# Kernel optimization log

Hardware: AMD Instinct MI355X
Metric: run time of the kernel (lower is better)

Reference implementation:

```python
import jax, jax.numpy as jnp
import numpy as np

N_STEPS = 20      # max(n_steps_al, n_steps_kc)
ALPHA   = 0.9     # membrane decay exp(-dt/tau_m)
V_TH    = 1.0     # spiking threshold
G_SOMA  = 0.3     # dendrite->axon coupling conductance (2-compartment KC)
APL_GAIN = 1.0    # graded APL gain
I_SCALE = 0.5     # graded ORN drive scale
BETA    = 10.0    # surrogate-gradient sharpness ('soft' sigmoid)

@jax.custom_vjp
def spike(x):
    return (x > 0).astype(x.dtype)

def _spike_fwd(x):
    return spike(x), x

def _spike_bwd(x, g):
    s = jax.nn.sigmoid(BETA * x)
    return (g * BETA * s * (1.0 - s),)

spike.defvjp(_spike_fwd, _spike_bwd)


def _sparse_w(key, shape, density):
    k1, k2 = jax.random.split(key)
    mask = jax.random.bernoulli(k1, density, shape)
    w = jax.random.uniform(k2, shape)
    return (mask * w).astype(jnp.float32)


def setup_inputs() -> dict:
    key = jax.random.key(0)
    ks = jax.random.split(key, 10)
    batch, n_or, n_orn, n_ln, n_pn, n_kc, n_odors = 4096, 21, 42, 56, 42, 2000, 34
    or_input = jax.random.uniform(ks[0], (batch, n_or), dtype=jnp.float32)
    or_gains = jnp.ones((n_or,), jnp.float32)
    # fixed OR->ORN mapping: OR i drives left (2i) and right (2i+1) ORNs
    m = np.zeros((n_or, n_orn), np.float32)
    for i in range(n_or):
        m[i, 2 * i] = 1.0
        m[i, 2 * i + 1] = 1.0
    mapping = jnp.asarray(m)
    orn_to_pn = _sparse_w(ks[1], (n_orn, n_pn), 0.3)
    orn_to_ln = _sparse_w(ks[2], (n_orn, n_ln), 0.3)
    ln_to_pn = _sparse_w(ks[3], (n_ln, n_pn), 0.3)
    pn_to_kc = _sparse_w(ks[4], (n_pn, n_kc), 0.15)  # ~6 PN claws per KC
    kc_to_apl = jax.random.uniform(ks[5], (n_kc, 1), dtype=jnp.float32) * 0.01
    apl_to_kc = jax.random.uniform(ks[6], (1, n_kc), dtype=jnp.float32)
    dec_w = jax.random.normal(ks[7], (n_kc, n_odors), dtype=jnp.float32) * 0.02
    dec_b = jnp.zeros((n_odors,), jnp.float32)
    return {"or_input": or_input, "or_gains": or_gains, "mapping": mapping,
            "orn_to_pn": orn_to_pn, "orn_to_ln": orn_to_ln, "ln_to_pn": ln_to_pn,
            "pn_to_kc": pn_to_kc, "kc_to_apl": kc_to_apl, "apl_to_kc": apl_to_kc,
            "dec_w": dec_w, "dec_b": dec_b}


def reference(or_input, or_gains, mapping, orn_to_pn, orn_to_ln, ln_to_pn,
              pn_to_kc, kc_to_apl, apl_to_kc, dec_w, dec_b):
    B = or_input.shape[0]
    n_orn, n_pn = orn_to_pn.shape
    n_ln = orn_to_ln.shape[1]
    n_kc = pn_to_kc.shape[1]
    # OR transduction: graded, learnable per-OR gain
    orn_drive = (or_input * jax.nn.softplus(or_gains)) @ mapping  # [B, n_orn]

    z = lambda n: jnp.zeros((B, n), or_input.dtype)
    carry0 = (z(n_orn), z(n_ln), z(n_pn), z(n_kc), z(n_kc), z(1), z(n_kc))

    def step(carry, _):
        v_orn, v_ln, v_pn, v_d, v_a, apl, kc_cnt = carry
        # ORN LIF driven by graded OR current
        v_orn = ALPHA * v_orn + I_SCALE * orn_drive
        s_orn = spike(v_orn - V_TH)
        v_orn = v_orn * (1.0 - s_orn)
        # LN LIF (lateral inhibition interneurons)
        v_ln = ALPHA * v_ln + s_orn @ orn_to_ln
        s_ln = spike(v_ln - V_TH)
        v_ln = v_ln * (1.0 - s_ln)
        # PN LIF: ORN excitation, LN inhibition
        v_pn = ALPHA * v_pn + s_orn @ orn_to_pn - s_ln @ ln_to_pn
        s_pn = spike(v_pn - V_TH)
        v_pn = v_pn * (1.0 - s_pn)
        # KC 2-compartment: dendrite gets PN input and APL inhibition
        v_d = ALPHA * v_d + s_pn @ pn_to_kc - apl @ apl_to_kc
        v_a = ALPHA * v_a + G_SOMA * (v_d - v_a)
        s_kc = spike(v_a - V_TH)
        v_a = v_a * (1.0 - s_kc)
        # APL: graded (non-spiking) global inhibition from KC spikes
        apl = APL_GAIN * jax.nn.relu(s_kc @ kc_to_apl)
        return (v_orn, v_ln, v_pn, v_d, v_a, apl, kc_cnt + s_kc), None

    carry, _ = jax.lax.scan(step, carry0, None, length=N_STEPS)
    kc_count = carry[-1]
    kc_rates = kc_count / N_STEPS
    logits = kc_rates @ dec_w + dec_b  # [B, n_odors]
    return logits
```

## Files before the change

### kernel.cpp

```cpp
#include <hip/hip_runtime.h>

#define NSTEPS 20
#define ALPHA  0.9f
#define VTH    1.0f
#define GSOMA  0.3f
#define ISCALE 0.5f

#define NOR  21
#define NORN 42
#define NLN  56
#define NPN  42
#define NKC  2000
#define NOD  34

#define TPB  256
#define KPER 8

__global__ __launch_bounds__(64)
void phase1a(const float* __restrict__ or_input,
             const float* __restrict__ or_gains,
             const float* __restrict__ mapping,
             const float* __restrict__ orn_to_ln,
             ulonglong2* __restrict__ gAB,
             int batch)
{
    const int lane = threadIdx.x;
    const int row  = blockIdx.x;
    if (row >= batch) return;

    const int jl = lane < NLN ? lane : 0;
    float wOl[NORN];
#pragma unroll
    for (int o = 0; o < NORN; ++o) wOl[o] = orn_to_ln[o * NLN + jl];

    float spg = 0.f;
    if (lane < NOR) spg = log1pf(expf(or_gains[lane]));

    float drive = 0.f;
    {
        const float* x = or_input + (long)row * NOR;
        const int jo = lane < NORN ? lane : 0;
#pragma unroll
        for (int i = 0; i < NOR; ++i) {
            float g = __shfl(spg, i);
            drive += x[i] * g * mapping[i * NORN + jo];
        }
        drive *= ISCALE;
    }

    float v_orn = 0.f, v_ln = 0.f;
    ulonglong2* outm = gAB + (long)row * NSTEPS;

    for (int t = 0; t < NSTEPS; ++t) {
        bool so = false;
        if (lane < NORN) {
            v_orn = ALPHA * v_orn + drive;
            so = (v_orn - VTH) > 0.f;
            if (so) v_orn = 0.f;
        }
        const unsigned long long mOrn = __ballot(so);
        const unsigned int mo_lo = (unsigned int)mOrn;
        const unsigned int mo_hi = (unsigned int)(mOrn >> 32);

        float aln = 0.f;
#pragma unroll
        for (int o = 0; o < 32; ++o) aln += (float)((mo_lo >> o) & 1u) * wOl[o];
#pragma unroll
        for (int o = 32; o < NORN; ++o) aln += (float)((mo_hi >> (o - 32)) & 1u) * wOl[o];

        bool sl = false;
        if (lane < NLN) {
            v_ln = ALPHA * v_ln + aln;
            sl = (v_ln - VTH) > 0.f;
            if (sl) v_ln = 0.f;
        }
        const unsigned long long mLn = __ballot(sl);
        if (lane == 0) outm[t] = make_ulonglong2(mOrn, mLn);
    }
}

__global__ __launch_bounds__(64)
void phase1b(const float* __restrict__ orn_to_pn,
             const float* __restrict__ ln_to_pn,
             const ulonglong2* __restrict__ gAB,
             unsigned long long* __restrict__ gPN,
             int batch)
{
    const int lane = threadIdx.x;
    const int row  = blockIdx.x;
    if (row >= batch) return;

    const int jp = lane < NPN ? lane : 0;
    float wOp[NORN], wLp[NLN];
#pragma unroll
    for (int o = 0; o < NORN; ++o) wOp[o] = orn_to_pn[o * NPN + jp];
#pragma unroll
    for (int l = 0; l < NLN; ++l) wLp[l] = ln_to_pn[l * NPN + jp];

    const ulonglong2* inm = gAB + (long)row * NSTEPS;
    unsigned long long* outm = gPN + (long)row * NSTEPS;

    float v_pn = 0.f;
    ulonglong2 ab = inm[0];

    for (int t = 0; t < NSTEPS; ++t) {
        ulonglong2 abn;
        if (t < NSTEPS - 1) abn = inm[t + 1];

        const unsigned int mo_lo = (unsigned int)ab.x;
        const unsigned int mo_hi = (unsigned int)(ab.x >> 32);
        const unsigned int ml_lo = (unsigned int)ab.y;
        const unsigned int ml_hi = (unsigned int)(ab.y >> 32);

        float apn = 0.f;
#pragma unroll
        for (int o = 0; o < 32; ++o) apn += (float)((mo_lo >> o) & 1u) * wOp[o];
#pragma unroll
        for (int o = 32; o < NORN; ++o) apn += (float)((mo_hi >> (o - 32)) & 1u) * wOp[o];

        float h = 0.f;
#pragma unroll
        for (int l = 0; l < 32; ++l) h += (float)((ml_lo >> l) & 1u) * wLp[l];
#pragma unroll
        for (int l = 32; l < NLN; ++l) h += (float)((ml_hi >> (l - 32)) & 1u) * wLp[l];

        bool sp = false;
        if (lane < NPN) {
            v_pn = ALPHA * v_pn + apn - h;
            sp = (v_pn - VTH) > 0.f;
            if (sp) v_pn = 0.f;
        }
        const unsigned long long mPn = __ballot(sp);
        if (lane == 0) outm[t] = mPn;
        ab = abn;
    }
}

__global__ __launch_bounds__(TPB)
void phase2_kernel(const unsigned long long* __restrict__ g_masks,
                   const float* __restrict__ pn_to_kc,
                   const float* __restrict__ kc_to_apl,
                   const float* __restrict__ apl_to_kc,
                   const float* __restrict__ dec_w,
                   const float* __restrict__ dec_b,
                   float* __restrict__ out)
{
    __shared__ float sRed[2][4];
    __shared__ float sRed2[4 * NOD];

    const int tid  = threadIdx.x;
    const int lane = tid & 63;
    const int wid  = tid >> 6;
    const int b    = blockIdx.x;

    const int  kbase = tid * KPER;
    const bool act   = (kbase < NKC);
    float vd[KPER], va[KPER], cnt[KPER], wa2k[KPER], wk2a[KPER];
#pragma unroll
    for (int j = 0; j < KPER; ++j) { vd[j] = 0.f; va[j] = 0.f; cnt[j] = 0.f; }
    {
        const float4* a4 = (const float4*)(apl_to_kc + (act ? kbase : 0));
        const float4* k4 = (const float4*)(kc_to_apl + (act ? kbase : 0));
        float4 a0 = a4[0], a1 = a4[1], k0 = k4[0], k1 = k4[1];
        const float g = act ? 1.f : 0.f;
        wa2k[0] = g * a0.x; wa2k[1] = g * a0.y; wa2k[2] = g * a0.z; wa2k[3] = g * a0.w;
        wa2k[4] = g * a1.x; wa2k[5] = g * a1.y; wa2k[6] = g * a1.z; wa2k[7] = g * a1.w;
        wk2a[0] = g * k0.x; wk2a[1] = g * k0.y; wk2a[2] = g * k0.z; wk2a[3] = g * k0.w;
        wk2a[4] = g * k1.x; wk2a[5] = g * k1.y; wk2a[6] = g * k1.z; wk2a[7] = g * k1.w;
    }
    if (tid < 8) sRed[tid >> 2][tid & 3] = 0.f;
    __syncthreads();

    const unsigned long long* gm = g_masks + (long)b * NSTEPS;

    for (int t = 0; t < NSTEPS; ++t) {
        const float* rp = sRed[(t + 1) & 1];
        const float apl = fmaxf(rp[0] + rp[1] + rp[2] + rp[3], 0.f);

#pragma unroll
        for (int j = 0; j < KPER; ++j) vd[j] = ALPHA * vd[j] - apl * wa2k[j];

        unsigned long long m = gm[t];
        while (m) {
            const int p0 = __builtin_ctzll(m); m &= m - 1;
            int p1 = p0; float f1 = 0.f;
            if (m) { p1 = __builtin_ctzll(m); m &= m - 1; f1 = 1.f; }
            if (act) {
                const float4* w0 = (const float4*)(pn_to_kc + (long)p0 * NKC + kbase);
                const float4* w1 = (const float4*)(pn_to_kc + (long)p1 * NKC + kbase);
                float4 a0 = w0[0], a1 = w0[1];
                float4 b0 = w1[0], b1 = w1[1];
                vd[0] += a0.x; vd[1] += a0.y; vd[2] += a0.z; vd[3] += a0.w;
                vd[4] += a1.x; vd[5] += a1.y; vd[6] += a1.z; vd[7] += a1.w;
                vd[0] += f1 * b0.x; vd[1] += f1 * b0.y; vd[2] += f1 * b0.z; vd[3] += f1 * b0.w;
                vd[4] += f1 * b1.x; vd[5] += f1 * b1.y; vd[6] += f1 * b1.z; vd[7] += f1 * b1.w;
            }
        }

        float aplp = 0.f;
#pragma unroll
        for (int j = 0; j < KPER; ++j) {
            va[j] = ALPHA * va[j] + GSOMA * (vd[j] - va[j]);
            float s = (va[j] - VTH) > 0.f ? 1.f : 0.f;
            va[j] *= (1.f - s);
            cnt[j] += s;
            aplp += s * wk2a[j];
        }
        for (int off = 32; off > 0; off >>= 1) aplp += __shfl_xor(aplp, off, 64);
        if (lane == 0) sRed[t & 1][wid] = aplp;
        __syncthreads();
    }

    float acc[NOD];
#pragma unroll
    for (int o = 0; o < NOD; ++o) acc[o] = 0.f;
    if (act) {
#pragma unroll
        for (int j = 0; j < KPER; ++j) {
            float r = cnt[j] / 20.0f;
            if (r != 0.f) {
                const float* wr = dec_w + (long)(kbase + j) * NOD;
#pragma unroll
                for (int o = 0; o < NOD; ++o) acc[o] += r * wr[o];
            }
        }
    }
#pragma unroll
    for (int o = 0; o < NOD; ++o) {
        float v = acc[o];
        for (int off = 32; off > 0; off >>= 1) v += __shfl_xor(v, off, 64);
        if (lane == 0) sRed2[wid * NOD + o] = v;
    }
    __syncthreads();
    if (tid < NOD) {
        float v = sRed2[tid] + sRed2[NOD + tid] + sRed2[2 * NOD + tid] +
                  sRed2[3 * NOD + tid] + dec_b[tid];
        out[(long)b * NOD + tid] = v;
    }
}

__global__ __launch_bounds__(TPB)
void snn_fused(const float* __restrict__ or_input, const float* __restrict__ or_gains,
               const float* __restrict__ mapping, const float* __restrict__ orn_to_pn,
               const float* __restrict__ orn_to_ln, const float* __restrict__ ln_to_pn,
               const float* __restrict__ pn_to_kc, const float* __restrict__ kc_to_apl,
               const float* __restrict__ apl_to_kc, const float* __restrict__ dec_w,
               const float* __restrict__ dec_b, float* __restrict__ out)
{
    __shared__ float sW_ol[NORN * NLN];
    __shared__ float sW_op[NORN * NPN];
    __shared__ float sW_lp[NLN * NPN];
    __shared__ float sDrive[NORN];
    __shared__ float sSpg[NOR];
    __shared__ float sOrn[NORN];
    __shared__ float sLn[NLN];
    __shared__ float sApl;
    __shared__ float sRed[4];
    __shared__ float sRed2[4 * NOD];
    __shared__ unsigned long long sMask;

    const int tid = threadIdx.x;
    const int b   = blockIdx.x;

    for (int i = tid; i < NORN * NLN; i += TPB) sW_ol[i] = orn_to_ln[i];
    for (int i = tid; i < NORN * NPN; i += TPB) sW_op[i] = orn_to_pn[i];
    for (int i = tid; i < NLN * NPN;  i += TPB) sW_lp[i] = ln_to_pn[i];
    if (tid < NOR) sSpg[tid] = log1pf(expf(or_gains[tid]));
    if (tid == 0)  sApl = 0.f;
    __syncthreads();

    if (tid < NORN) {
        const float* x = or_input + (long)b * NOR;
        float d = 0.f;
        for (int i = 0; i < NOR; ++i) d += x[i] * sSpg[i] * mapping[i * NORN + tid];
        sDrive[tid] = d * ISCALE;
    }

    const int  kbase = tid * KPER;
    const bool act   = (kbase < NKC);
    float vd[KPER], va[KPER], cnt[KPER], wa2k[KPER], wk2a[KPER];
#pragma unroll
    for (int j = 0; j < KPER; ++j) {
        vd[j] = 0.f; va[j] = 0.f; cnt[j] = 0.f;
        wa2k[j] = act ? apl_to_kc[kbase + j] : 0.f;
        wk2a[j] = act ? kc_to_apl[kbase + j] : 0.f;
    }
    float v_orn = 0.f, v_ln = 0.f, v_pn = 0.f, v_pn_exc = 0.f;
    __syncthreads();

    for (int t = 0; t < NSTEPS; ++t) {
        if (tid < NORN) {
            v_orn = ALPHA * v_orn + sDrive[tid];
            float s = (v_orn - VTH) > 0.f ? 1.f : 0.f;
            v_orn *= (1.f - s);
            sOrn[tid] = s;
        }
        __syncthreads();
        if (tid < NLN) {
            float a = 0.f;
            for (int o = 0; o < NORN; ++o) a += sOrn[o] * sW_ol[o * NLN + tid];
            v_ln = ALPHA * v_ln + a;
            float s = (v_ln - VTH) > 0.f ? 1.f : 0.f;
            v_ln *= (1.f - s);
            sLn[tid] = s;
        } else if (tid >= 64 && tid < 64 + NPN) {
            const int j = tid - 64;
            float a = 0.f;
            for (int o = 0; o < NORN; ++o) a += sOrn[o] * sW_op[o * NPN + j];
            v_pn_exc = a;
        }
        __syncthreads();
        if (tid >= 64 && tid < 64 + NPN) {
            const int j = tid - 64;
            float inh = 0.f;
            for (int l = 0; l < NLN; ++l) inh += sLn[l] * sW_lp[l * NPN + j];
            v_pn = ALPHA * v_pn + v_pn_exc - inh;
            bool s = (v_pn - VTH) > 0.f;
            if (s) v_pn = 0.f;
            unsigned long long bal = __ballot(s);
            if (tid == 64) sMask = bal;
        }
        __syncthreads();
        {
            const float apl = sApl;
#pragma unroll
            for (int j = 0; j < KPER; ++j) vd[j] = ALPHA * vd[j] - apl * wa2k[j];
            unsigned long long m = sMask;
            while (m) {
                const int p = __builtin_ctzll(m);
                m &= m - 1;
                if (act) {
                    const float4* w = (const float4*)(pn_to_kc + (long)p * NKC + kbase);
                    float4 w0 = w[0], w1 = w[1];
                    vd[0] += w0.x; vd[1] += w0.y; vd[2] += w0.z; vd[3] += w0.w;
                    vd[4] += w1.x; vd[5] += w1.y; vd[6] += w1.z; vd[7] += w1.w;
                }
            }
            float aplp = 0.f;
#pragma unroll
            for (int j = 0; j < KPER; ++j) {
                va[j] = ALPHA * va[j] + GSOMA * (vd[j] - va[j]);
                float s = (va[j] - VTH) > 0.f ? 1.f : 0.f;
                va[j] *= (1.f - s);
                cnt[j] += s;
                aplp += s * wk2a[j];
            }
            for (int off = 32; off > 0; off >>= 1) aplp += __shfl_xor(aplp, off, 64);
            if ((tid & 63) == 0) sRed[tid >> 6] = aplp;
        }
        __syncthreads();
        if (tid == 0) {
            float a = sRed[0] + sRed[1] + sRed[2] + sRed[3];
            sApl = fmaxf(a, 0.f);
        }
    }

    float acc[NOD];
#pragma unroll
    for (int o = 0; o < NOD; ++o) acc[o] = 0.f;
    if (act) {
#pragma unroll
        for (int j = 0; j < KPER; ++j) {
            float r = cnt[j] / 20.0f;
            if (r != 0.f) {
                const float* wr = dec_w + (long)(kbase + j) * NOD;
#pragma unroll
                for (int o = 0; o < NOD; ++o) acc[o] += r * wr[o];
            }
        }
    }
#pragma unroll
    for (int o = 0; o < NOD; ++o) {
        float v = acc[o];
        for (int off = 32; off > 0; off >>= 1) v += __shfl_xor(v, off, 64);
        if ((tid & 63) == 0) sRed2[(tid >> 6) * NOD + o] = v;
    }
    __syncthreads();
    if (tid < NOD) {
        float v = sRed2[tid] + sRed2[NOD + tid] + sRed2[2 * NOD + tid] +
                  sRed2[3 * NOD + tid] + dec_b[tid];
        out[(long)b * NOD + tid] = v;
    }
}

extern "C" void kernel_launch(void* const* d_in, const int* in_sizes, int n_in,
                              void* d_out, int out_size, void* d_ws, size_t ws_size,
                              hipStream_t stream) {
    (void)n_in; (void)out_size;
    const float* or_input  = (const float*)d_in[0];
    const float* or_gains  = (const float*)d_in[1];
    const float* mapping   = (const float*)d_in[2];
    const float* orn_to_pn = (const float*)d_in[3];
    const float* orn_to_ln = (const float*)d_in[4];
    const float* ln_to_pn  = (const float*)d_in[5];
    const float* pn_to_kc  = (const float*)d_in[6];
    const float* kc_to_apl = (const float*)d_in[7];
    const float* apl_to_kc = (const float*)d_in[8];
    const float* dec_w     = (const float*)d_in[9];
    const float* dec_b     = (const float*)d_in[10];
    float* out = (float*)d_out;

    const int batch = in_sizes[0] / NOR;
    const size_t needAB = (size_t)batch * NSTEPS * sizeof(ulonglong2);
    const size_t needPN = (size_t)batch * NSTEPS * sizeof(unsigned long long);

    if (ws_size >= needAB + needPN) {
        ulonglong2* gAB = (ulonglong2*)d_ws;
        unsigned long long* gPN = (unsigned long long*)((char*)d_ws + needAB);
        hipLaunchKernelGGL(phase1a, dim3(batch), dim3(64), 0, stream,
                           or_input, or_gains, mapping, orn_to_ln, gAB, batch);
        hipLaunchKernelGGL(phase1b, dim3(batch), dim3(64), 0, stream,
                           orn_to_pn, ln_to_pn, gAB, gPN, batch);
        hipLaunchKernelGGL(phase2_kernel, dim3(batch), dim3(TPB), 0, stream,
                           gPN, pn_to_kc, kc_to_apl, apl_to_kc, dec_w, dec_b, out);
    } else {
        hipLaunchKernelGGL(snn_fused, dim3(batch), dim3(TPB), 0, stream,
                           or_input, or_gains, mapping, orn_to_pn, orn_to_ln,
                           ln_to_pn, pn_to_kc, kc_to_apl, apl_to_kc, dec_w, dec_b, out);
    }
}
```

Measured before the change: 209.7 us.

## Fuse ORN/LN and PN phase kernels and process two batch rows per wavefront

Merges the two phase-1 kernels into one, so the ORN and LN spike masks stay in registers instead of being written to and reread from the workspace. Each 64-lane block now handles two batch rows, which amortizes the weight loads into registers and gives the serial dependency chain more independent work to interleave. The cost is higher register pressure (about 140 weight floats plus duplicated state), which may reduce occupancy. The number of blocks is also halved.

After: 228.6 us. 1.09x slower.

```diff
diff --git a/kernel.cpp b/kernel.cpp
--- a/kernel.cpp
+++ b/kernel.cpp
@@ -17,122 +17,131 @@
 #define KPER 8
 
 __global__ __launch_bounds__(64)
-void phase1a(const float* __restrict__ or_input,
-             const float* __restrict__ or_gains,
-             const float* __restrict__ mapping,
-             const float* __restrict__ orn_to_ln,
-             ulonglong2* __restrict__ gAB,
-             int batch)
+void phase1_fused(const float* __restrict__ or_input,
+                  const float* __restrict__ or_gains,
+                  const float* __restrict__ mapping,
+                  const float* __restrict__ orn_to_ln,
+                  const float* __restrict__ orn_to_pn,
+                  const float* __restrict__ ln_to_pn,
+                  unsigned long long* __restrict__ gPN,
+                  int batch)
 {
     const int lane = threadIdx.x;
-    const int row  = blockIdx.x;
-    if (row >= batch) return;
+    const int rowA = blockIdx.x * 2;
+    if (rowA >= batch) return;
+    const int rowB = rowA + 1;
+    const bool hasB = rowB < batch;
 
     const int jl = lane < NLN ? lane : 0;
-    float wOl[NORN];
+    const int jp = lane < NPN ? lane : 0;
+
+    float wOl[NORN], wOp[NORN], wLp[NLN];
 #pragma unroll
     for (int o = 0; o < NORN; ++o) wOl[o] = orn_to_ln[o * NLN + jl];
+#pragma unroll
+    for (int o = 0; o < NORN; ++o) wOp[o] = orn_to_pn[o * NPN + jp];
+#pragma unroll
+    for (int l = 0; l < NLN; ++l) wLp[l] = ln_to_pn[l * NPN + jp];
 
     float spg = 0.f;
     if (lane < NOR) spg = log1pf(expf(or_gains[lane]));
 
-    float drive = 0.f;
+    float driveA = 0.f, driveB = 0.f;
     {
-        const float* x = or_input + (long)row * NOR;
+        const float* xA = or_input + (long)rowA * NOR;
+        const float* xB = or_input + (long)(hasB ? rowB : rowA) * NOR;
         const int jo = lane < NORN ? lane : 0;
 #pragma unroll
         for (int i = 0; i < NOR; ++i) {
             float g = __shfl(spg, i);
-            drive += x[i] * g * mapping[i * NORN + jo];
-        }
-        drive *= ISCALE;
-    }
-
-    float v_orn = 0.f, v_ln = 0.f;
-    ulonglong2* outm = gAB + (long)row * NSTEPS;
+            float m = mapping[i * NORN + jo];
+            driveA += xA[i] * g * m;
+            driveB += xB[i] * g * m;
+        }
+        driveA *= ISCALE;
+        driveB *= ISCALE;
+    }
+
+    float voA = 0.f, voB = 0.f, vlA = 0.f, vlB = 0.f, vpA = 0.f, vpB = 0.f;
+    unsigned long long* outA = gPN + (long)rowA * NSTEPS;
+    unsigned long long* outB = gPN + (long)rowB * NSTEPS;
 
     for (int t = 0; t < NSTEPS; ++t) {
-        bool so = false;
+        bool soA = false, soB = false;
         if (lane < NORN) {
-            v_orn = ALPHA * v_orn + drive;
-            so = (v_orn - VTH) > 0.f;
-            if (so) v_orn = 0.f;
-        }
-        const unsigned long long mOrn = __ballot(so);
-        const unsigned int mo_lo = (unsigned int)mOrn;
-        const unsigned int mo_hi = (unsigned int)(mOrn >> 32);
-
-        float aln = 0.f;
-#pragma unroll
-        for (int o = 0; o < 32; ++o) aln += (float)((mo_lo >> o) & 1u) * wOl[o];
-#pragma unroll
-        for (int o = 32; o < NORN; ++o) aln += (float)((mo_hi >> (o - 32)) & 1u) * wOl[o];
-
-        bool sl = false;
+            voA = ALPHA * voA + driveA;
+            soA = (voA - VTH) > 0.f;
+            if (soA) voA = 0.f;
+            voB = ALPHA * voB + driveB;
+            soB = (voB - VTH) > 0.f;
+            if (soB) voB = 0.f;
+        }
+        const unsigned long long mOA = __ballot(soA);
+        const unsigned long long mOB = __ballot(soB);
+        const unsigned int aol = (unsigned int)mOA, aoh = (unsigned int)(mOA >> 32);
+        const unsigned int bol = (unsigned int)mOB, boh = (unsigned int)(mOB >> 32);
+
+        float alnA = 0.f, alnB = 0.f;
+#pragma unroll
+        for (int o = 0; o < 32; ++o) {
+            alnA += (float)((aol >> o) & 1u) * wOl[o];
+            alnB += (float)((bol >> o) & 1u) * wOl[o];
+        }
+#pragma unroll
+        for (int o = 32; o < NORN; ++o) {
+            alnA += (float)((aoh >> (o - 32)) & 1u) * wOl[o];
+            alnB += (float)((boh >> (o - 32)) & 1u) * wOl[o];
+        }
+        bool slA = false, slB = false;
         if (lane < NLN) {
-            v_ln = ALPHA * v_ln + aln;
-            sl = (v_ln - VTH) > 0.f;
-            if (sl) v_ln = 0.f;
-        }
-        const unsigned long long mLn = __ballot(sl);
-        if (lane == 0) outm[t] = make_ulonglong2(mOrn, mLn);
-    }
-}
-
-__global__ __launch_bounds__(64)
-void phase1b(const float* __restrict__ orn_to_pn,
-             const float* __restrict__ ln_to_pn,
-             const ulonglong2* __restrict__ gAB,
-             unsigned long long* __restrict__ gPN,
-             int batch)
-{
-    const int lane = threadIdx.x;
-    const int row  = blockIdx.x;
-    if (row >= batch) return;
-
-    const int jp = lane < NPN ? lane : 0;
-    float wOp[NORN], wLp[NLN];
-#pragma unroll
-    for (int o = 0; o < NORN; ++o) wOp[o] = orn_to_pn[o * NPN + jp];
-#pragma unroll
-    for (int l = 0; l < NLN; ++l) wLp[l] = ln_to_pn[l * NPN + jp];
-
-    const ulonglong2* inm = gAB + (long)row * NSTEPS;
-    unsigned long long* outm = gPN + (long)row * NSTEPS;
-
-    float v_pn = 0.f;
-    ulonglong2 ab = inm[0];
-
-    for (int t = 0; t < NSTEPS; ++t) {
-        ulonglong2 abn;
-        if (t < NSTEPS - 1) abn = inm[t + 1];
-
-        const unsigned int mo_lo = (unsigned int)ab.x;
-        const unsigned int mo_hi = (unsigned int)(ab.x >> 32);
-        const unsigned int ml_lo = (unsigned int)ab.y;
-        const unsigned int ml_hi = (unsigned int)(ab.y >> 32);
-
-        float apn = 0.f;
-#pragma unroll
-        for (int o = 0; o < 32; ++o) apn += (float)((mo_lo >> o) & 1u) * wOp[o];
-#pragma unroll
-        for (int o = 32; o < NORN; ++o) apn += (float)((mo_hi >> (o - 32)) & 1u) * wOp[o];
-
-        float h = 0.f;
-#pragma unroll
-        for (int l = 0; l < 32; ++l) h += (float)((ml_lo >> l) & 1u) * wLp[l];
-#pragma unroll
-        for (int l = 32; l < NLN; ++l) h += (float)((ml_hi >> (l - 32)) & 1u) * wLp[l];
-
-        bool sp = false;
+            vlA = ALPHA * vlA + alnA;
+            slA = (vlA - VTH) > 0.f;
+            if (slA) vlA = 0.f;
+            vlB = ALPHA * vlB + alnB;
+            slB = (vlB - VTH) > 0.f;
+            if (slB) vlB = 0.f;
+        }
+        const unsigned long long mLA = __ballot(slA);
+        const unsigned long long mLB = __ballot(slB);
+        const unsigned int all_ = (unsigned int)mLA, alh = (unsigned int)(mLA >> 32);
+        const unsigned int bll = (unsigned int)mLB, blh = (unsigned int)(mLB >> 32);
+
+        float apnA = 0.f, apnB = 0.f;
+#pragma unroll
+        for (int o = 0; o < 32; ++o) {
+            apnA += (float)((aol >> o) & 1u) * wOp[o];
+            apnB += (float)((bol >> o) & 1u) * wOp[o];
+        }
+#pragma unroll
+        for (int o = 32; o < NORN; ++o) {
+            apnA += (float)((aoh >> (o - 32)) & 1u) * wOp[o];
+            apnB += (float)((boh >> (o - 32)) & 1u) * wOp[o];
+        }
+        float hA = 0.f, hB = 0.f;
+#pragma unroll
+        for (int l = 0; l < 32; ++l) {
+            hA += (float)((all_ >> l) & 1u) * wLp[l];
+            hB += (float)((bll >> l) & 1u) * wLp[l];
+        }
+#pragma unroll
+        for (int l = 32; l < NLN; ++l) {
+            hA += (float)((alh >> (l - 32)) & 1u) * wLp[l];
+            hB += (float)((blh >> (l - 32)) & 1u) * wLp[l];
+        }
+
+        bool spA = false, spB = false;
         if (lane < NPN) {
-            v_pn = ALPHA * v_pn + apn - h;
-            sp = (v_pn - VTH) > 0.f;
-            if (sp) v_pn = 0.f;
-        }
-        const unsigned long long mPn = __ballot(sp);
-        if (lane == 0) outm[t] = mPn;
-        ab = abn;
+            vpA = ALPHA * vpA + apnA - hA;
+            spA = (vpA - VTH) > 0.f;
+            if (spA) vpA = 0.f;
+            vpB = ALPHA * vpB + apnB - hB;
+            spB = (vpB - VTH) > 0.f;
+            if (spB) vpB = 0.f;
+        }
+        const unsigned long long mPA = __ballot(spA);
+        const unsigned long long mPB = __ballot(spB);
+        if (lane == 0) outA[t] = mPA;
+        if (lane == 1 && hasB) outB[t] = mPB;
     }
 }
 
@@ -401,16 +410,13 @@
     float* out = (float*)d_out;
 
     const int batch = in_sizes[0] / NOR;
-    const size_t needAB = (size_t)batch * NSTEPS * sizeof(ulonglong2);
     const size_t needPN = (size_t)batch * NSTEPS * sizeof(unsigned long long);
 
-    if (ws_size >= needAB + needPN) {
-        ulonglong2* gAB = (ulonglong2*)d_ws;
-        unsigned long long* gPN = (unsigned long long*)((char*)d_ws + needAB);
-        hipLaunchKernelGGL(phase1a, dim3(batch), dim3(64), 0, stream,
-                           or_input, or_gains, mapping, orn_to_ln, gAB, batch);
-        hipLaunchKernelGGL(phase1b, dim3(batch), dim3(64), 0, stream,
-                           orn_to_pn, ln_to_pn, gAB, gPN, batch);
+    if (ws_size >= needPN) {
+        unsigned long long* gPN = (unsigned long long*)d_ws;
+        hipLaunchKernelGGL(phase1_fused, dim3((batch + 1) / 2), dim3(64), 0, stream,
+                           or_input, or_gains, mapping, orn_to_ln, orn_to_pn, ln_to_pn,
+                           gPN, batch);
         hipLaunchKernelGGL(phase2_kernel, dim3(batch), dim3(TPB), 0, stream,
                            gPN, pn_to_kc, kc_to_apl, apl_to_kc, dec_w, dec_b, out);
     } else {
```

## Fuse ORN/LN and PN phases into one kernel with sparse spike iteration

Applied to the files above, without the earlier changes.

Merges the two phase-1 kernels into one, so the intermediate ORN/LN spike masks no longer make a round trip through global memory. Weights are staged in shared memory, and each block handles four batch rows, one per wavefront. The dense per-bit multiply-accumulate loops are replaced with loops that visit only the set bits of the spike ballot. This cuts launch overhead, traffic and arithmetic, but brings divergence-free yet data-dependent loop lengths and some LDS bank traffic.

New measurement: 224.1 us. +6.9%, slower.

```diff
diff --git a/kernel.cpp b/kernel.cpp
--- a/kernel.cpp
+++ b/kernel.cpp
@@ -16,22 +16,30 @@
 #define TPB  256
 #define KPER 8
 
-__global__ __launch_bounds__(64)
-void phase1a(const float* __restrict__ or_input,
-             const float* __restrict__ or_gains,
-             const float* __restrict__ mapping,
-             const float* __restrict__ orn_to_ln,
-             ulonglong2* __restrict__ gAB,
-             int batch)
+__global__ __launch_bounds__(TPB)
+void phase1_sparse(const float* __restrict__ or_input,
+                   const float* __restrict__ or_gains,
+                   const float* __restrict__ mapping,
+                   const float* __restrict__ orn_to_ln,
+                   const float* __restrict__ orn_to_pn,
+                   const float* __restrict__ ln_to_pn,
+                   unsigned long long* __restrict__ gPN,
+                   int batch)
 {
-    const int lane = threadIdx.x;
-    const int row  = blockIdx.x;
+    __shared__ float sOl[NORN * NLN];
+    __shared__ float sOp[NORN * NPN];
+    __shared__ float sLp[NLN * NPN];
+
+    const int tid = threadIdx.x;
+    for (int i = tid; i < NORN * NLN; i += TPB) sOl[i] = orn_to_ln[i];
+    for (int i = tid; i < NORN * NPN; i += TPB) sOp[i] = orn_to_pn[i];
+    for (int i = tid; i < NLN * NPN;  i += TPB) sLp[i] = ln_to_pn[i];
+    __syncthreads();
+
+    const int lane = tid & 63;
+    const int wid  = tid >> 6;
+    const int row  = blockIdx.x * 4 + wid;
     if (row >= batch) return;
-
-    const int jl = lane < NLN ? lane : 0;
-    float wOl[NORN];
-#pragma unroll
-    for (int o = 0; o < NORN; ++o) wOl[o] = orn_to_ln[o * NLN + jl];
 
     float spg = 0.f;
     if (lane < NOR) spg = log1pf(expf(or_gains[lane]));
@@ -48,8 +56,11 @@
         drive *= ISCALE;
     }
 
-    float v_orn = 0.f, v_ln = 0.f;
-    ulonglong2* outm = gAB + (long)row * NSTEPS;
+    const int jl = lane < NLN ? lane : 0;
+    const int jp = lane < NPN ? lane : 0;
+
+    float v_orn = 0.f, v_ln = 0.f, v_pn = 0.f;
+    unsigned long long* outm = gPN + (long)row * NSTEPS;
 
     for (int t = 0; t < NSTEPS; ++t) {
         bool so = false;
@@ -58,15 +69,18 @@
             so = (v_orn - VTH) > 0.f;
             if (so) v_orn = 0.f;
         }
-        const unsigned long long mOrn = __ballot(so);
-        const unsigned int mo_lo = (unsigned int)mOrn;
-        const unsigned int mo_hi = (unsigned int)(mOrn >> 32);
-
-        float aln = 0.f;
-#pragma unroll
-        for (int o = 0; o < 32; ++o) aln += (float)((mo_lo >> o) & 1u) * wOl[o];
-#pragma unroll
-        for (int o = 32; o < NORN; ++o) aln += (float)((mo_hi >> (o - 32)) & 1u) * wOl[o];
+        unsigned long long mO = __ballot(so);
+
+        float aln = 0.f, apn = 0.f;
+        {
+            unsigned long long m = mO;
+            while (m) {
+                const int p = __builtin_ctzll(m);
+                m &= m - 1;
+                aln += sOl[p * NLN + jl];
+                apn += sOp[p * NPN + jp];
+            }
+        }
 
         bool sl = false;
         if (lane < NLN) {
@@ -74,55 +88,17 @@
             sl = (v_ln - VTH) > 0.f;
             if (sl) v_ln = 0.f;
         }
-        const unsigned long long mLn = __ballot(sl);
-        if (lane == 0) outm[t] = make_ulonglong2(mOrn, mLn);
-    }
-}
-
-__global__ __launch_bounds__(64)
-void phase1b(const float* __restrict__ orn_to_pn,
-             const float* __restrict__ ln_to_pn,
-             const ulonglong2* __restrict__ gAB,
-             unsigned long long* __restrict__ gPN,
-             int batch)
-{
-    const int lane = threadIdx.x;
-    const int row  = blockIdx.x;
-    if (row >= batch) return;
-
-    const int jp = lane < NPN ? lane : 0;
-    float wOp[NORN], wLp[NLN];
-#pragma unroll
-    for (int o = 0; o < NORN; ++o) wOp[o] = orn_to_pn[o * NPN + jp];
-#pragma unroll
-    for (int l = 0; l < NLN; ++l) wLp[l] = ln_to_pn[l * NPN + jp];
-
-    const ulonglong2* inm = gAB + (long)row * NSTEPS;
-    unsigned long long* outm = gPN + (long)row * NSTEPS;
-
-    float v_pn = 0.f;
-    ulonglong2 ab = inm[0];
-
-    for (int t = 0; t < NSTEPS; ++t) {
-        ulonglong2 abn;
-        if (t < NSTEPS - 1) abn = inm[t + 1];
-
-        const unsigned int mo_lo = (unsigned int)ab.x;
-        const unsigned int mo_hi = (unsigned int)(ab.x >> 32);
-        const unsigned int ml_lo = (unsigned int)ab.y;
-        const unsigned int ml_hi = (unsigned int)(ab.y >> 32);
-
-        float apn = 0.f;
-#pragma unroll
-        for (int o = 0; o < 32; ++o) apn += (float)((mo_lo >> o) & 1u) * wOp[o];
-#pragma unroll
-        for (int o = 32; o < NORN; ++o) apn += (float)((mo_hi >> (o - 32)) & 1u) * wOp[o];
+        unsigned long long mL = __ballot(sl);
 
         float h = 0.f;
-#pragma unroll
-        for (int l = 0; l < 32; ++l) h += (float)((ml_lo >> l) & 1u) * wLp[l];
-#pragma unroll
-        for (int l = 32; l < NLN; ++l) h += (float)((ml_hi >> (l - 32)) & 1u) * wLp[l];
+        {
+            unsigned long long m = mL;
+            while (m) {
+                const int l = __builtin_ctzll(m);
+                m &= m - 1;
+                h += sLp[l * NPN + jp];
+            }
+        }
 
         bool sp = false;
         if (lane < NPN) {
@@ -130,9 +106,8 @@
             sp = (v_pn - VTH) > 0.f;
             if (sp) v_pn = 0.f;
         }
-        const unsigned long long mPn = __ballot(sp);
-        if (lane == 0) outm[t] = mPn;
-        ab = abn;
+        const unsigned long long mP = __ballot(sp);
+        if (lane == 0) outm[t] = mP;
     }
 }
 
@@ -401,16 +376,13 @@
     float* out = (float*)d_out;
 
     const int batch = in_sizes[0] / NOR;
-    const size_t needAB = (size_t)batch * NSTEPS * sizeof(ulonglong2);
     const size_t needPN = (size_t)batch * NSTEPS * sizeof(unsigned long long);
 
-    if (ws_size >= needAB + needPN) {
-        ulonglong2* gAB = (ulonglong2*)d_ws;
-        unsigned long long* gPN = (unsigned long long*)((char*)d_ws + needAB);
-        hipLaunchKernelGGL(phase1a, dim3(batch), dim3(64), 0, stream,
-                           or_input, or_gains, mapping, orn_to_ln, gAB, batch);
-        hipLaunchKernelGGL(phase1b, dim3(batch), dim3(64), 0, stream,
-                           orn_to_pn, ln_to_pn, gAB, gPN, batch);
+    if (ws_size >= needPN) {
+        unsigned long long* gPN = (unsigned long long*)d_ws;
+        hipLaunchKernelGGL(phase1_sparse, dim3((batch + 3) / 4), dim3(TPB), 0, stream,
+                           or_input, or_gains, mapping, orn_to_ln, orn_to_pn, ln_to_pn,
+                           gPN, batch);
         hipLaunchKernelGGL(phase2_kernel, dim3(batch), dim3(TPB), 0, stream,
                            gPN, pn_to_kc, kc_to_apl, apl_to_kc, dec_w, dec_b, out);
     } else {
```

## Process two batch samples per block in KC phase to halve barriers

Applied to the files above, without the earlier changes.

The KC-phase kernel now handles two batch rows per 256-thread block, interleaving their per-step updates and sharing one __syncthreads per timestep plus the shared weight registers. The aim is to amortize the per-step block barrier and APL reduction latency over two samples and expose more independent work for latency hiding. In exchange it roughly doubles per-thread state registers (and the decoder accumulator phase), which may reduce occupancy, and it halves the grid size.

Result: slower. 222.7 us (+6.2%).

```diff
diff --git a/kernel.cpp b/kernel.cpp
--- a/kernel.cpp
+++ b/kernel.cpp
@@ -137,30 +137,40 @@
 }
 
 __global__ __launch_bounds__(TPB)
-void phase2_kernel(const unsigned long long* __restrict__ g_masks,
-                   const float* __restrict__ pn_to_kc,
-                   const float* __restrict__ kc_to_apl,
-                   const float* __restrict__ apl_to_kc,
-                   const float* __restrict__ dec_w,
-                   const float* __restrict__ dec_b,
-                   float* __restrict__ out)
+void phase2_dual(const unsigned long long* __restrict__ g_masks,
+                 const float* __restrict__ pn_to_kc,
+                 const float* __restrict__ kc_to_apl,
+                 const float* __restrict__ apl_to_kc,
+                 const float* __restrict__ dec_w,
+                 const float* __restrict__ dec_b,
+                 float* __restrict__ out,
+                 int batch)
 {
-    __shared__ float sRed[2][4];
-    __shared__ float sRed2[4 * NOD];
+    __shared__ float sRedA[2][4];
+    __shared__ float sRedB[2][4];
+    __shared__ float sRed2[2][4 * NOD];
 
     const int tid  = threadIdx.x;
     const int lane = tid & 63;
     const int wid  = tid >> 6;
-    const int b    = blockIdx.x;
+    const int bA   = blockIdx.x * 2;
+    const int bB   = bA + 1;
+    const bool hasB = (bB < batch);
 
     const int  kbase = tid * KPER;
     const bool act   = (kbase < NKC);
-    float vd[KPER], va[KPER], cnt[KPER], wa2k[KPER], wk2a[KPER];
-#pragma unroll
-    for (int j = 0; j < KPER; ++j) { vd[j] = 0.f; va[j] = 0.f; cnt[j] = 0.f; }
+    float vdA[KPER], vaA[KPER], cntA[KPER];
+    float vdB[KPER], vaB[KPER], cntB[KPER];
+    float wa2k[KPER], wk2a[KPER];
+#pragma unroll
+    for (int j = 0; j < KPER; ++j) {
+        vdA[j] = 0.f; vaA[j] = 0.f; cntA[j] = 0.f;
+        vdB[j] = 0.f; vaB[j] = 0.f; cntB[j] = 0.f;
+    }
     {
-        const float4* a4 = (const float4*)(apl_to_kc + (act ? kbase : 0));
-        const float4* k4 = (const float4*)(kc_to_apl + (act ? kbase : 0));
+        const int idx = act ? kbase : 0;
+        const float4* a4 = (const float4*)(apl_to_kc + idx);
+        const float4* k4 = (const float4*)(kc_to_apl + idx);
         float4 a0 = a4[0], a1 = a4[1], k0 = k4[0], k1 = k4[1];
         const float g = act ? 1.f : 0.f;
         wa2k[0] = g * a0.x; wa2k[1] = g * a0.y; wa2k[2] = g * a0.z; wa2k[3] = g * a0.w;
@@ -168,74 +178,143 @@
         wk2a[0] = g * k0.x; wk2a[1] = g * k0.y; wk2a[2] = g * k0.z; wk2a[3] = g * k0.w;
         wk2a[4] = g * k1.x; wk2a[5] = g * k1.y; wk2a[6] = g * k1.z; wk2a[7] = g * k1.w;
     }
-    if (tid < 8) sRed[tid >> 2][tid & 3] = 0.f;
+    if (tid < 8) {
+        sRedA[tid >> 2][tid & 3] = 0.f;
+        sRedB[tid >> 2][tid & 3] = 0.f;
+    }
     __syncthreads();
 
-    const unsigned long long* gm = g_masks + (long)b * NSTEPS;
+    const unsigned long long* gmA = g_masks + (long)bA * NSTEPS;
+    const unsigned long long* gmB = g_masks + (long)(hasB ? bB : bA) * NSTEPS;
 
     for (int t = 0; t < NSTEPS; ++t) {
-        const float* rp = sRed[(t + 1) & 1];
-        const float apl = fmaxf(rp[0] + rp[1] + rp[2] + rp[3], 0.f);
-
-#pragma unroll
-        for (int j = 0; j < KPER; ++j) vd[j] = ALPHA * vd[j] - apl * wa2k[j];
-
-        unsigned long long m = gm[t];
-        while (m) {
-            const int p0 = __builtin_ctzll(m); m &= m - 1;
-            int p1 = p0; float f1 = 0.f;
-            if (m) { p1 = __builtin_ctzll(m); m &= m - 1; f1 = 1.f; }
-            if (act) {
-                const float4* w0 = (const float4*)(pn_to_kc + (long)p0 * NKC + kbase);
-                const float4* w1 = (const float4*)(pn_to_kc + (long)p1 * NKC + kbase);
-                float4 a0 = w0[0], a1 = w0[1];
-                float4 b0 = w1[0], b1 = w1[1];
-                vd[0] += a0.x; vd[1] += a0.y; vd[2] += a0.z; vd[3] += a0.w;
-                vd[4] += a1.x; vd[5] += a1.y; vd[6] += a1.z; vd[7] += a1.w;
-                vd[0] += f1 * b0.x; vd[1] += f1 * b0.y; vd[2] += f1 * b0.z; vd[3] += f1 * b0.w;
-                vd[4] += f1 * b1.x; vd[5] += f1 * b1.y; vd[6] += f1 * b1.z; vd[7] += f1 * b1.w;
-            }
-        }
-
-        float aplp = 0.f;
-#pragma unroll
-        for (int j = 0; j < KPER; ++j) {
-            va[j] = ALPHA * va[j] + GSOMA * (vd[j] - va[j]);
-            float s = (va[j] - VTH) > 0.f ? 1.f : 0.f;
-            va[j] *= (1.f - s);
-            cnt[j] += s;
-            aplp += s * wk2a[j];
-        }
-        for (int off = 32; off > 0; off >>= 1) aplp += __shfl_xor(aplp, off, 64);
-        if (lane == 0) sRed[t & 1][wid] = aplp;
+        {
+            const float* rp = sRedA[(t + 1) & 1];
+            const float apl = fmaxf(rp[0] + rp[1] + rp[2] + rp[3], 0.f);
+#pragma unroll
+            for (int j = 0; j < KPER; ++j) vdA[j] = ALPHA * vdA[j] - apl * wa2k[j];
+
+            unsigned long long m = gmA[t];
+            while (m) {
+                const int p0 = __builtin_ctzll(m); m &= m - 1;
+                int p1 = p0; float f1 = 0.f;
+                if (m) { p1 = __builtin_ctzll(m); m &= m - 1; f1 = 1.f; }
+                if (act) {
+                    const float4* w0 = (const float4*)(pn_to_kc + (long)p0 * NKC + kbase);
+                    const float4* w1 = (const float4*)(pn_to_kc + (long)p1 * NKC + kbase);
+                    float4 a0 = w0[0], a1 = w0[1];
+                    float4 b0 = w1[0], b1 = w1[1];
+                    vdA[0] += a0.x; vdA[1] += a0.y; vdA[2] += a0.z; vdA[3] += a0.w;
+                    vdA[4] += a1.x; vdA[5] += a1.y; vdA[6] += a1.z; vdA[7] += a1.w;
+                    vdA[0] += f1 * b0.x; vdA[1] += f1 * b0.y; vdA[2] += f1 * b0.z; vdA[3] += f1 * b0.w;
+                    vdA[4] += f1 * b1.x; vdA[5] += f1 * b1.y; vdA[6] += f1 * b1.z; vdA[7] += f1 * b1.w;
+                }
+            }
+
+            float aplp = 0.f;
+#pragma unroll
+            for (int j = 0; j < KPER; ++j) {
+                vaA[j] = ALPHA * vaA[j] + GSOMA * (vdA[j] - vaA[j]);
+                float s = (vaA[j] - VTH) > 0.f ? 1.f : 0.f;
+                vaA[j] *= (1.f - s);
+                cntA[j] += s;
+                aplp += s * wk2a[j];
+            }
+            for (int off = 32; off > 0; off >>= 1) aplp += __shfl_xor(aplp, off, 64);
+            if (lane == 0) sRedA[t & 1][wid] = aplp;
+        }
+        {
+            const float* rp = sRedB[(t + 1) & 1];
+            const float apl = fmaxf(rp[0] + rp[1] + rp[2] + rp[3], 0.f);
+#pragma unroll
+            for (int j = 0; j < KPER; ++j) vdB[j] = ALPHA * vdB[j] - apl * wa2k[j];
+
+            unsigned long long m = gmB[t];
+            while (m) {
+                const int p0 = __builtin_ctzll(m); m &= m - 1;
+                int p1 = p0; float f1 = 0.f;
+                if (m) { p1 = __builtin_ctzll(m); m &= m - 1; f1 = 1.f; }
+                if (act) {
+                    const float4* w0 = (const float4*)(pn_to_kc + (long)p0 * NKC + kbase);
+                    const float4* w1 = (const float4*)(pn_to_kc + (long)p1 * NKC + kbase);
+                    float4 a0 = w0[0], a1 = w0[1];
+                    float4 b0 = w1[0], b1 = w1[1];
+                    vdB[0] += a0.x; vdB[1] += a0.y; vdB[2] += a0.z; vdB[3] += a0.w;
+                    vdB[4] += a1.x; vdB[5] += a1.y; vdB[6] += a1.z; vdB[7] += a1.w;
+                    vdB[0] += f1 * b0.x; vdB[1] += f1 * b0.y; vdB[2] += f1 * b0.z; vdB[3] += f1 * b0.w;
+                    vdB[4] += f1 * b1.x; vdB[5] += f1 * b1.y; vdB[6] += f1 * b1.z; vdB[7] += f1 * b1.w;
+                }
+            }
+
+            float aplp = 0.f;
+#pragma unroll
+            for (int j = 0; j < KPER; ++j) {
+                vaB[j] = ALPHA * vaB[j] + GSOMA * (vdB[j] - vaB[j]);
+                float s = (vaB[j] - VTH) > 0.f ? 1.f : 0.f;
+                vaB[j] *= (1.f - s);
+                cntB[j] += s;
+                aplp += s * wk2a[j];
+            }
+            for (int off = 32; off > 0; off >>= 1) aplp += __shfl_xor(aplp, off, 64);
+            if (lane == 0) sRedB[t & 1][wid] = aplp;
+        }
         __syncthreads();
     }
 
-    float acc[NOD];
-#pragma unroll
-    for (int o = 0; o < NOD; ++o) acc[o] = 0.f;
-    if (act) {
-#pragma unroll
-        for (int j = 0; j < KPER; ++j) {
-            float r = cnt[j] / 20.0f;
-            if (r != 0.f) {
-                const float* wr = dec_w + (long)(kbase + j) * NOD;
-#pragma unroll
-                for (int o = 0; o < NOD; ++o) acc[o] += r * wr[o];
-            }
-        }
-    }
-#pragma unroll
-    for (int o = 0; o < NOD; ++o) {
-        float v = acc[o];
-        for (int off = 32; off > 0; off >>= 1) v += __shfl_xor(v, off, 64);
-        if (lane == 0) sRed2[wid * NOD + o] = v;
+    {
+        float acc[NOD];
+#pragma unroll
+        for (int o = 0; o < NOD; ++o) acc[o] = 0.f;
+        if (act) {
+#pragma unroll
+            for (int j = 0; j < KPER; ++j) {
+                float r = cntA[j] / 20.0f;
+                if (r != 0.f) {
+                    const float* wr = dec_w + (long)(kbase + j) * NOD;
+#pragma unroll
+                    for (int o = 0; o < NOD; ++o) acc[o] += r * wr[o];
+                }
+            }
+        }
+#pragma unroll
+        for (int o = 0; o < NOD; ++o) {
+            float v = acc[o];
+            for (int off = 32; off > 0; off >>= 1) v += __shfl_xor(v, off, 64);
+            if (lane == 0) sRed2[0][wid * NOD + o] = v;
+        }
+    }
+    {
+        float acc[NOD];
+#pragma unroll
+        for (int o = 0; o < NOD; ++o) acc[o] = 0.f;
+        if (act) {
+#pragma unroll
+            for (int j = 0; j < KPER; ++j) {
+                float r = cntB[j] / 20.0f;
+                if (r != 0.f) {
+                    const float* wr = dec_w + (long)(kbase + j) * NOD;
+#pragma unroll
+                    for (int o = 0; o < NOD; ++o) acc[o] += r * wr[o];
+                }
+            }
+        }
+#pragma unroll
+        for (int o = 0; o < NOD; ++o) {
+            float v = acc[o];
+            for (int off = 32; off > 0; off >>= 1) v += __shfl_xor(v, off, 64);
+            if (lane == 0) sRed2[1][wid * NOD + o] = v;
+        }
     }
     __syncthreads();
     if (tid < NOD) {
-        float v = sRed2[tid] + sRed2[NOD + tid] + sRed2[2 * NOD + tid] +
-                  sRed2[3 * NOD + tid] + dec_b[tid];
-        out[(long)b * NOD + tid] = v;
+        float v = sRed2[0][tid] + sRed2[0][NOD + tid] + sRed2[0][2 * NOD + tid] +
+                  sRed2[0][3 * NOD + tid] + dec_b[tid];
+        out[(long)bA * NOD + tid] = v;
+    } else if (tid >= 64 && tid < 64 + NOD && hasB) {
+        const int o = tid - 64;
+        float v = sRed2[1][o] + sRed2[1][NOD + o] + sRed2[1][2 * NOD + o] +
+                  sRed2[1][3 * NOD + o] + dec_b[o];
+        out[(long)bB * NOD + o] = v;
     }
 }
 
@@ -411,8 +490,8 @@
                            or_input, or_gains, mapping, orn_to_ln, gAB, batch);
         hipLaunchKernelGGL(phase1b, dim3(batch), dim3(64), 0, stream,
                            orn_to_pn, ln_to_pn, gAB, gPN, batch);
-        hipLaunchKernelGGL(phase2_kernel, dim3(batch), dim3(TPB), 0, stream,
-                           gPN, pn_to_kc, kc_to_apl, apl_to_kc, dec_w, dec_b, out);
+        hipLaunchKernelGGL(phase2_dual, dim3((batch + 1) / 2), dim3(TPB), 0, stream,
+                           gPN, pn_to_kc, kc_to_apl, apl_to_kc, dec_w, dec_b, out, batch);
     } else {
         hipLaunchKernelGGL(snn_fused, dim3(batch), dim3(TPB), 0, stream,
                            or_input, or_gains, mapping, orn_to_pn, orn_to_ln,
```
